# Kernel tuning notes

Measured on AMD Instinct MI355X. Metric: run time of the kernel, lower is better.

The kernel has to match this reference:

```python
import jax, jax.numpy as jnp
import numpy as np

D_MODEL = 1024
D_HEAD = 64
MAX_REL = 8
B, T = 4, 4096


def setup_inputs() -> dict:
    key = jax.random.key(0)
    k1, k2, k3, k4, k5 = jax.random.split(key, 5)
    return {
        "x": jax.random.normal(k1, (B, T, D_MODEL), dtype=jnp.float32),
        "W_q": jax.random.normal(k2, (D_HEAD, D_MODEL), dtype=jnp.float32) * (1.0 / np.sqrt(D_MODEL)),
        "W_k": jax.random.normal(k3, (D_HEAD, D_MODEL), dtype=jnp.float32) * (1.0 / np.sqrt(D_MODEL)),
        "W_v": jax.random.normal(k4, (D_HEAD, D_MODEL), dtype=jnp.float32) * (1.0 / np.sqrt(D_MODEL)),
        "rel_emb": jax.random.normal(k5, (2 * MAX_REL + 1, 1), dtype=jnp.float32),
    }


def reference(x, W_q, W_k, W_v, rel_emb):
    Bb, Tt, _ = x.shape
    scale = jnp.sqrt(jnp.asarray(W_q.shape[0], dtype=x.dtype))
    # projections (Linear: x @ W.T)
    q = jnp.einsum("btd,hd->bth", x, W_q)
    k = jnp.einsum("btd,hd->bth", x, W_k)
    v = jnp.einsum("btd,hd->bth", x, W_v)
    scores = jnp.einsum("bth,bsh->bts", q, k) / scale  # [B,T,T]
    # relative position bias: rel_emb[clip(j-i, -M, M) + M]
    i_idx = jnp.arange(Tt)[:, None]
    j_idx = jnp.arange(Tt)[None, :]
    rel = jnp.clip(j_idx - i_idx, -MAX_REL, MAX_REL) + MAX_REL  # [T,T] int
    rel_bias = rel_emb[rel, 0]  # [T,T]
    scores = scores + rel_bias[None, :, :]
    causal = j_idx <= i_idx  # [T,T] lower-triangular
    scores = jnp.where(causal[None, :, :], scores, -jnp.inf)
    attn = jax.nn.softmax(scores, axis=-1)
    return jnp.einsum("bts,bsh->bth", attn, v)
```

## Files before the change

### kernel.cpp

```cpp
#include <hip/hip_runtime.h>
#include <hip/hip_bf16.h>

#define BT 4
#define TT 4096
#define DM 1024
#define DH 64
#define NRE 17
#define LOG2E 1.4426950408889634f

using bf16 = __hip_bfloat16;
typedef __attribute__((ext_vector_type(8))) short short8;
typedef __attribute__((ext_vector_type(4))) short short4v;
typedef __attribute__((ext_vector_type(4))) float float4v;

#define BC8(x) __builtin_bit_cast(short8, x)

static __device__ __forceinline__ short8 load8(const bf16* p) {
    return *reinterpret_cast<const short8*>(p);
}
static __device__ __forceinline__ short bfbits(float x) {
    return (short)__bfloat16_as_ushort(__float2bfloat16(x));
}
static __device__ __forceinline__ short8 pack8(float4v a, float4v b) {
    short8 r;
    r[0] = bfbits(a[0]); r[1] = bfbits(a[1]); r[2] = bfbits(a[2]); r[3] = bfbits(a[3]);
    r[4] = bfbits(b[0]); r[5] = bfbits(b[1]); r[6] = bfbits(b[2]); r[7] = bfbits(b[3]);
    return r;
}
static __device__ __forceinline__ void gload_lds16(const void* g, void* l) {
    __builtin_amdgcn_global_load_lds(
        (const __attribute__((address_space(1))) void*)g,
        (__attribute__((address_space(3))) void*)l, 16, 0, 0);
}
static __device__ __forceinline__ unsigned lds_addr(const void* p) {
    return (unsigned)(size_t)(const __attribute__((address_space(3))) void*)p;
}

#define DSR(dst, addr, off) \
    asm volatile("ds_read_b128 %0, %1 offset:" off : "=v"(dst) : "v"(addr))


__global__ __launch_bounds__(256) void w_prep(
    const float* __restrict__ Wq, const float* __restrict__ Wk,
    const float* __restrict__ Wv, bf16* __restrict__ Wswz)
{
    const unsigned g = blockIdx.x * 256 + threadIdx.x;
    const unsigned c    = g / 768;
    const unsigned rem  = g - c * 768;
    const unsigned pair = rem >> 3;
    const unsigned slot = rem & 7;
    const unsigned l    = slot ^ (pair & 7);
    const unsigned row  = 2 * pair + (l >> 2);
    const unsigned k    = 32 * c + (l & 3) * 8;
    const float* src = (row < 64) ? &Wq[(size_t)row * DM + k]
                     : (row < 128) ? &Wk[(size_t)(row - 64) * DM + k]
                                   : &Wv[(size_t)(row - 128) * DM + k];
    float4v a = *reinterpret_cast<const float4v*>(src);
    float4v b = *reinterpret_cast<const float4v*>(src + 4);
    *reinterpret_cast<short8*>(&Wswz[(size_t)g * 8]) = pack8(a, b);
}

__global__ __launch_bounds__(256, 2) void qkv_gemm(
    const float* __restrict__ x, const bf16* __restrict__ Wswz,
    bf16* __restrict__ Qb, bf16* __restrict__ Kswz, bf16* __restrict__ Vswz)
{
    __shared__ __align__(16) float xs[2][2048];
    __shared__ __align__(16) short Wls[2][12288];

    const int w    = threadIdx.x >> 6;
    const int lane = threadIdx.x & 63;
    const int quad = lane >> 4;
    const int l16  = lane & 15;
    const int half = w & 1;
    const int colh = w >> 1;
    const int row0 = blockIdx.x * 32;

    float4v acc[6];
#pragma unroll
    for (int i = 0; i < 6; i++) acc[i] = (float4v)(0.f);

    auto stage = [&](int c, int p) {
#pragma unroll
        for (int j = 0; j < 2; j++) {
            const int call = 2 * w + j;
            const int row  = 4 * call + (lane >> 4);
            const int pu   = lane & 15;
            const int gu   = (pu & 8) | ((pu ^ row) & 7);
            gload_lds16(&x[(size_t)(row0 + row) * DM + c * 64 + gu * 4],
                        &xs[p][call * 256]);
        }
#pragma unroll
        for (int j = 0; j < 6; j++) {
            const int call = 6 * w + j;
            gload_lds16(&Wswz[(size_t)(2 * c) * 6144 + call * 512 + lane * 8],
                        &Wls[p][call * 512]);
        }
    };

    const unsigned xlds = lds_addr(&xs[0][0]);
    const unsigned wlds = lds_addr(&Wls[0][0]);
    const int R        = 16 * half + l16;
    const int lo3_0    = (2 * quad)     ^ (R & 7);
    const int lo3_1    = (2 * quad + 1) ^ (R & 7);
    const int pairBase = 48 * colh + (l16 >> 1);
    const int physW    = ((l16 & 1) * 4 + quad) ^ ((l16 >> 1) & 7);

    stage(0, 0);

    for (int c = 0; c < 16; c++) {
        const int p = c & 1;
        __syncthreads();
        if (c + 1 < 16) stage(c + 1, p ^ 1);

        const unsigned xb  = xlds + (unsigned)(p * 8192) + R * 64 * 4;
        const unsigned xa0 = xb + lo3_0 * 16;
        const unsigned xa1 = xb + lo3_1 * 16;
        const unsigned wa  = wlds + (unsigned)(p * 24576) + pairBase * 128 + physW * 16;

        float4v x00, x01, x10, x11;
        float4v w00, w01, w02, w03, w04, w05, w10, w11, w12, w13, w14, w15;
        DSR(x00, xa0, "0");   DSR(x10, xa0, "128");
        DSR(x01, xa1, "0");   DSR(x11, xa1, "128");
        DSR(w00, wa, "0");     DSR(w01, wa, "1024");  DSR(w02, wa, "2048");
        DSR(w03, wa, "3072");  DSR(w04, wa, "4096");  DSR(w05, wa, "5120");
        DSR(w10, wa, "12288"); DSR(w11, wa, "13312"); DSR(w12, wa, "14336");
        DSR(w13, wa, "15360"); DSR(w14, wa, "16384"); DSR(w15, wa, "17408");
        asm volatile("s_waitcnt lgkmcnt(0)"
            : "+v"(x00), "+v"(x01), "+v"(x10), "+v"(x11),
              "+v"(w00), "+v"(w01), "+v"(w02), "+v"(w03), "+v"(w04), "+v"(w05),
              "+v"(w10), "+v"(w11), "+v"(w12), "+v"(w13), "+v"(w14), "+v"(w15));

        short8 a0 = pack8(x00, x01);
        short8 a1 = pack8(x10, x11);
        acc[0] = __builtin_amdgcn_mfma_f32_16x16x32_bf16(a0, BC8(w00), acc[0], 0, 0, 0);
        acc[1] = __builtin_amdgcn_mfma_f32_16x16x32_bf16(a0, BC8(w01), acc[1], 0, 0, 0);
        acc[2] = __builtin_amdgcn_mfma_f32_16x16x32_bf16(a0, BC8(w02), acc[2], 0, 0, 0);
        acc[3] = __builtin_amdgcn_mfma_f32_16x16x32_bf16(a0, BC8(w03), acc[3], 0, 0, 0);
        acc[4] = __builtin_amdgcn_mfma_f32_16x16x32_bf16(a0, BC8(w04), acc[4], 0, 0, 0);
        acc[5] = __builtin_amdgcn_mfma_f32_16x16x32_bf16(a0, BC8(w05), acc[5], 0, 0, 0);
        acc[0] = __builtin_amdgcn_mfma_f32_16x16x32_bf16(a1, BC8(w10), acc[0], 0, 0, 0);
        acc[1] = __builtin_amdgcn_mfma_f32_16x16x32_bf16(a1, BC8(w11), acc[1], 0, 0, 0);
        acc[2] = __builtin_amdgcn_mfma_f32_16x16x32_bf16(a1, BC8(w12), acc[2], 0, 0, 0);
        acc[3] = __builtin_amdgcn_mfma_f32_16x16x32_bf16(a1, BC8(w13), acc[3], 0, 0, 0);
        acc[4] = __builtin_amdgcn_mfma_f32_16x16x32_bf16(a1, BC8(w14), acc[4], 0, 0, 0);
        acc[5] = __builtin_amdgcn_mfma_f32_16x16x32_bf16(a1, BC8(w15), acc[5], 0, 0, 0);
    }

    __syncthreads();
    short* Kimg = (short*)&xs[0][0];
    short* Vimg = Kimg + 2048;
#pragma unroll
    for (int nt = 0; nt < 6; nt++) {
        const int cc = 96 * colh + 16 * nt + l16;
#pragma unroll
        for (int r = 0; r < 4; r++) {
            const int jl = 16 * half + 4 * quad + r;
            const short hb = bfbits(acc[nt][r]);
            if (cc < 64) {
                Qb[(size_t)(row0 + jl) * DH + cc] = __hip_bfloat16_raw{(unsigned short)hb};
            } else if (cc < 128) {
                const int k  = cc - 64;
                const int h  = k >> 5;
                const int q2 = (k & 31) >> 3;
                Kimg[((2 * half + h) * 64 + q2 * 16 + 4 * quad + r) * 8 + (k & 7)] = hb;
            } else {
                const int d  = cc - 128;
                const int dh = d >> 5;
                const int hi = (d >> 4) & 1;
                Vimg[((2 * half + dh) * 64 + quad * 16 + (d & 15)) * 8 + hi * 4 + r] = hb;
            }
        }
    }
    __syncthreads();
    {
        const int b_     = row0 >> 12;
        const int tile32 = (row0 & (TT - 1)) >> 5;
        const size_t base = ((size_t)(b_ * 512 + tile32 * 4)) * 512;
        const int u = threadIdx.x;
        *reinterpret_cast<short8*>(&Kswz[base + (size_t)u * 8]) =
            *reinterpret_cast<const short8*>(&Kimg[u * 8]);
        *reinterpret_cast<short8*>(&Vswz[base + (size_t)u * 8]) =
            *reinterpret_cast<const short8*>(&Vimg[u * 8]);
    }
}

__global__ __launch_bounds__(512, 2) void attn(
    const bf16* __restrict__ Qb, const bf16* __restrict__ Kswz,
    const bf16* __restrict__ Vswz, const float* __restrict__ rel,
    float* __restrict__ out)
{
    __shared__ __align__(16) short sbuf[32768];

    const int w     = threadIdx.x >> 6;
    const int lane  = threadIdx.x & 63;
    const int quad  = lane >> 4;
    const int l16   = lane & 15;
    const int batch = blockIdx.x & 3;
    const int pr    = blockIdx.x >> 2;

    const float SCL = 0.125f * LOG2E;
    float relreg = 0.f;
    if (lane < NRE) relreg = rel[lane] * LOG2E;
    const float rel0 = __shfl(relreg, 0, 64);

    const size_t bbase = (size_t)batch * TT;

    short* mybuf = &sbuf[w * 4096];
    const unsigned sbase = lds_addr(&sbuf[0]) + (unsigned)(w * 8192 + lane * 16);

    float* Osh = (float*)&sbuf[0];
    float* mM  = Osh + 4 * 32 * 68;
    float* lL  = mM + 256;

    auto stageKV = [&](int T) {
        const size_t gb = ((size_t)(batch * 512 + T * 4)) * 512;
#pragma unroll
        for (int j = 0; j < 4; j++)
            gload_lds16(&Kswz[gb + j * 512 + lane * 8], mybuf + j * 512);
#pragma unroll
        for (int j = 0; j < 4; j++)
            gload_lds16(&Vswz[gb + j * 512 + lane * 8], mybuf + 2048 + j * 512);
    };

#pragma unroll 1
    for (int ph = 0; ph < 2; ph++) {
        const int t  = ph ? (127 - pr) : pr;
        const int q0 = 32 * t;

        short8 bq[2][2];
#pragma unroll
        for (int qh = 0; qh < 2; qh++) {
            const bf16* qp = &Qb[(bbase + q0 + 16 * qh + l16) * DH];
            bq[qh][0] = load8(qp + quad * 8);
            bq[qh][1] = load8(qp + 32 + quad * 8);
        }
        __builtin_amdgcn_s_waitcnt(0xF70);

        float4v o[2][4];
#pragma unroll
        for (int qh = 0; qh < 2; qh++)
#pragma unroll
            for (int dt = 0; dt < 4; dt++) o[qh][dt] = (float4v)(0.f);
        float m_st[2] = {-1e30f, -1e30f}, l_st[2] = {0.f, 0.f};

        const int cnt = (t >= w) ? (((t - w) >> 3) + 1) : 0;
        if (cnt > 0) stageKV(w);

        for (int k = 0; k < cnt; k++) {
            const int T = w + 8 * k;
            __builtin_amdgcn_s_waitcnt(0xF70);

            float4v kf0, kf1, kf2, kf3, vf0, vf1, vf2, vf3;
            DSR(kf0, sbase, "0");    DSR(kf1, sbase, "1024");
            DSR(kf2, sbase, "2048"); DSR(kf3, sbase, "3072");
            DSR(vf0, sbase, "4096"); DSR(vf1, sbase, "5120");
            DSR(vf2, sbase, "6144"); DSR(vf3, sbase, "7168");
            asm volatile("s_waitcnt lgkmcnt(0)"
                : "+v"(kf0), "+v"(kf1), "+v"(kf2), "+v"(kf3),
                  "+v"(vf0), "+v"(vf1), "+v"(vf2), "+v"(vf3));

            if (k + 1 < cnt) stageKV(w + 8 * (k + 1));

            const int js = 32 * T;
#pragma unroll
            for (int qh = 0; qh < 2; qh++) {
                float4v st[2];
                st[0] = (float4v)(0.f); st[1] = (float4v)(0.f);
                __builtin_amdgcn_s_setprio(1);
                st[0] = __builtin_amdgcn_mfma_f32_16x16x32_bf16(BC8(kf0), bq[qh][0], st[0], 0, 0, 0);
                st[0] = __builtin_amdgcn_mfma_f32_16x16x32_bf16(BC8(kf1), bq[qh][1], st[0], 0, 0, 0);
                st[1] = __builtin_amdgcn_mfma_f32_16x16x32_bf16(BC8(kf2), bq[qh][0], st[1], 0, 0, 0);
                st[1] = __builtin_amdgcn_mfma_f32_16x16x32_bf16(BC8(kf3), bq[qh][1], st[1], 0, 0, 0);
                __builtin_amdgcn_s_setprio(0);

                const int i_row = q0 + 16 * qh + l16;
                float mcur = -1e30f;
                if (js + 40 <= q0 + 16 * qh) {
#pragma unroll
                    for (int n = 0; n < 2; n++)
#pragma unroll
                        for (int r = 0; r < 4; r++) {
                            float v = st[n][r] * SCL + rel0;
                            st[n][r] = v;
                            mcur = fmaxf(mcur, v);
                        }
                } else {
#pragma unroll
                    for (int n = 0; n < 2; n++) {
                        const int jb = js + 16 * n + 4 * quad;
#pragma unroll
                        for (int r = 0; r < 4; r++) {
                            const int d = jb + r - i_row;
                            int idx = d + 8;
                            idx = idx < 0 ? 0 : (idx > 16 ? 16 : idx);
                            float v = st[n][r] * SCL + __shfl(relreg, idx, 64);
                            v = (d > 0) ? -1e30f : v;
                            st[n][r] = v;
                            mcur = fmaxf(mcur, v);
                        }
                    }
                }

                mcur = fmaxf(mcur, __shfl_xor(mcur, 16, 64));
                mcur = fmaxf(mcur, __shfl_xor(mcur, 32, 64));

                if (__any(mcur > m_st[qh] + 8.f)) {
                    const float mn = fmaxf(m_st[qh], mcur);
                    const float alpha = exp2f(m_st[qh] - mn);
                    m_st[qh] = mn;
                    l_st[qh] *= alpha;
#pragma unroll
                    for (int dt = 0; dt < 4; dt++)
#pragma unroll
                        for (int r = 0; r < 4; r++) o[qh][dt][r] *= alpha;
                }
                const float mn = m_st[qh];

                float lsum = 0.f;
                short4v pb[2];
#pragma unroll
                for (int n = 0; n < 2; n++)
#pragma unroll
                    for (int r = 0; r < 4; r++) {
                        const float e = exp2f(st[n][r] - mn);
                        lsum += e;
                        pb[n][r] = bfbits(e);
                    }
                lsum += __shfl_xor(lsum, 16, 64);
                lsum += __shfl_xor(lsum, 32, 64);
                l_st[qh] += lsum;

                __builtin_amdgcn_s_setprio(1);
#pragma unroll
                for (int n = 0; n < 2; n++) {
#pragma unroll
                    for (int dh = 0; dh < 2; dh++) {
                        const short8 vs = BC8((dh == 0) ? ((n == 0) ? vf0 : vf2)
                                                        : ((n == 0) ? vf1 : vf3));
                        short4v lo, hi;
                        lo[0] = vs[0]; lo[1] = vs[1]; lo[2] = vs[2]; lo[3] = vs[3];
                        hi[0] = vs[4]; hi[1] = vs[5]; hi[2] = vs[6]; hi[3] = vs[7];
                        o[qh][2 * dh]     = __builtin_amdgcn_mfma_f32_16x16x16bf16_1k(lo, pb[n], o[qh][2 * dh], 0, 0, 0);
                        o[qh][2 * dh + 1] = __builtin_amdgcn_mfma_f32_16x16x16bf16_1k(hi, pb[n], o[qh][2 * dh + 1], 0, 0, 0);
                    }
                }
                __builtin_amdgcn_s_setprio(0);
            }
        }

        __syncthreads();
        if (w >= 4) {
            const int slot = w - 4;
#pragma unroll
            for (int qh = 0; qh < 2; qh++) {
                const int row = 16 * qh + l16;
                if (quad == 0) { mM[w * 32 + row] = m_st[qh]; lL[w * 32 + row] = l_st[qh]; }
#pragma unroll
                for (int dt = 0; dt < 4; dt++)
                    *reinterpret_cast<float4v*>(&Osh[(slot * 32 + row) * 68 + 16 * dt + 4 * quad]) = o[qh][dt];
            }
        }
        __syncthreads();
        if (w < 4) {
#pragma unroll
            for (int qh = 0; qh < 2; qh++) {
                const int row = 16 * qh + l16;
                const float mp = mM[(w + 4) * 32 + row], lp = lL[(w + 4) * 32 + row];
                const float M  = fmaxf(m_st[qh], mp);
                const float ea = exp2f(m_st[qh] - M);
                const float eb = exp2f(mp - M);
                const float ln = l_st[qh] * ea + lp * eb;
#pragma unroll
                for (int dt = 0; dt < 4; dt++) {
                    float4v op = *reinterpret_cast<float4v*>(&Osh[(w * 32 + row) * 68 + 16 * dt + 4 * quad]);
#pragma unroll
                    for (int r = 0; r < 4; r++) o[qh][dt][r] = o[qh][dt][r] * ea + op[r] * eb;
                }
                if (quad == 0) { mM[w * 32 + row] = M; lL[w * 32 + row] = ln; }
#pragma unroll
                for (int dt = 0; dt < 4; dt++)
                    *reinterpret_cast<float4v*>(&Osh[(w * 32 + row) * 68 + 16 * dt + 4 * quad]) = o[qh][dt];
            }
        }
        __syncthreads();
        {
            for (int idx = threadIdx.x; idx < 32 * 64; idx += 512) {
                const int row = idx >> 6;
                const int col = idx & 63;
                float M = mM[row];
#pragma unroll
                for (int s = 1; s < 4; s++) M = fmaxf(M, mM[s * 32 + row]);
                float L = 0.f, a = 0.f;
#pragma unroll
                for (int s = 0; s < 4; s++) {
                    const float ex = exp2f(mM[s * 32 + row] - M);
                    L += lL[s * 32 + row] * ex;
                    a += Osh[(s * 32 + row) * 68 + col] * ex;
                }
                out[(bbase + q0 + row) * DH + col] = a / L;
            }
        }
        __syncthreads();
    }
}

extern "C" void kernel_launch(void* const* d_in, const int* in_sizes, int n_in,
                              void* d_out, int out_size, void* d_ws, size_t ws_size,
                              hipStream_t stream)
{
    const float* x   = (const float*)d_in[0];
    const float* Wq  = (const float*)d_in[1];
    const float* Wk  = (const float*)d_in[2];
    const float* Wv  = (const float*)d_in[3];
    const float* rel = (const float*)d_in[4];
    float* out = (float*)d_out;

    bf16* Qb   = (bf16*)d_ws;
    bf16* Kswz = Qb   + (size_t)BT * TT * DH;
    bf16* Vswz = Kswz + (size_t)BT * TT * DH;
    bf16* Wswz = Vswz + (size_t)BT * TT * DH;

    w_prep<<<96, 256, 0, stream>>>(Wq, Wk, Wv, Wswz);
    qkv_gemm<<<512, 256, 0, stream>>>(x, Wswz, Qb, Kswz, Vswz);
    attn<<<256, 512, 0, stream>>>(Qb, Kswz, Vswz, rel, out);
}
```

Before: 147.6 us.

## Split attention KV range across two blocks and merge partials in a new kernel

The attention grid is doubled so that each query tile is handled by two blocks, each covering alternating KV tiles (stride 16 instead of 8). One half writes unnormalized partial output directly to out, the other to a workspace buffer, and both save per-row max and sum. A new merge kernel combines the two halves with log-sum-exp rescaling. This gives more parallelism and better occupancy across CUs, at the cost of an extra kernel launch and extra global traffic for the partials.

```diff
diff --git a/kernel.cpp b/kernel.cpp
--- a/kernel.cpp
+++ b/kernel.cpp
@@ -187,7 +187,7 @@
 __global__ __launch_bounds__(512, 2) void attn(
     const bf16* __restrict__ Qb, const bf16* __restrict__ Kswz,
     const bf16* __restrict__ Vswz, const float* __restrict__ rel,
-    float* __restrict__ out)
+    float* __restrict__ out, float* __restrict__ part1, float* __restrict__ msl)
 {
     __shared__ __align__(16) short sbuf[32768];
 
@@ -196,7 +196,10 @@
     const int quad  = lane >> 4;
     const int l16   = lane & 15;
     const int batch = blockIdx.x & 3;
-    const int pr    = blockIdx.x >> 2;
+    const int rest  = blockIdx.x >> 2;
+    const int pr    = rest >> 1;
+    const int hh    = rest & 1;
+    const int s     = w + 8 * hh;
 
     const float SCL = 0.125f * LOG2E;
     float relreg = 0.f;
@@ -243,11 +246,11 @@
             for (int dt = 0; dt < 4; dt++) o[qh][dt] = (float4v)(0.f);
         float m_st[2] = {-1e30f, -1e30f}, l_st[2] = {0.f, 0.f};
 
-        const int cnt = (t >= w) ? (((t - w) >> 3) + 1) : 0;
-        if (cnt > 0) stageKV(w);
+        const int cnt = (t >= s) ? (((t - s) >> 4) + 1) : 0;
+        if (cnt > 0) stageKV(s);
 
         for (int k = 0; k < cnt; k++) {
-            const int T = w + 8 * k;
+            const int T = s + 16 * k;
             __builtin_amdgcn_s_waitcnt(0xF70);
 
             float4v kf0, kf1, kf2, kf3, vf0, vf1, vf2, vf3;
@@ -259,7 +262,7 @@
                 : "+v"(kf0), "+v"(kf1), "+v"(kf2), "+v"(kf3),
                   "+v"(vf0), "+v"(vf1), "+v"(vf2), "+v"(vf3));
 
-            if (k + 1 < cnt) stageKV(w + 8 * (k + 1));
+            if (k + 1 < cnt) stageKV(s + 16 * (k + 1));
 
             const int js = 32 * T;
 #pragma unroll
@@ -384,23 +387,50 @@
         }
         __syncthreads();
         {
+            const int q = batch * 128 + t;
+            float* ob = hh ? (part1 + (size_t)q * 2048)
+                           : (out + ((size_t)bbase + q0) * DH);
+            float* ml = msl + (size_t)(q * 2 + hh) * 64;
             for (int idx = threadIdx.x; idx < 32 * 64; idx += 512) {
                 const int row = idx >> 6;
                 const int col = idx & 63;
                 float M = mM[row];
 #pragma unroll
-                for (int s = 1; s < 4; s++) M = fmaxf(M, mM[s * 32 + row]);
+                for (int s2 = 1; s2 < 4; s2++) M = fmaxf(M, mM[s2 * 32 + row]);
                 float L = 0.f, a = 0.f;
 #pragma unroll
-                for (int s = 0; s < 4; s++) {
-                    const float ex = exp2f(mM[s * 32 + row] - M);
-                    L += lL[s * 32 + row] * ex;
-                    a += Osh[(s * 32 + row) * 68 + col] * ex;
+                for (int s2 = 0; s2 < 4; s2++) {
+                    const float ex = exp2f(mM[s2 * 32 + row] - M);
+                    L += lL[s2 * 32 + row] * ex;
+                    a += Osh[(s2 * 32 + row) * 68 + col] * ex;
                 }
-                out[(bbase + q0 + row) * DH + col] = a / L;
+                ob[idx] = a;
+                if (col == 0) { ml[row] = M; ml[32 + row] = L; }
             }
         }
         __syncthreads();
+    }
+}
+
+__global__ __launch_bounds__(256) void attn_merge(
+    const float* __restrict__ part1, const float* __restrict__ msl,
+    float* __restrict__ out)
+{
+    const int q = blockIdx.x;
+    const int batch = q >> 7, t = q & 127;
+    float* ob0 = out + ((size_t)batch * TT + t * 32) * DH;
+    const float* o1  = part1 + (size_t)q * 2048;
+    const float* ml0 = msl + (size_t)(q * 2 + 0) * 64;
+    const float* ml1 = msl + (size_t)(q * 2 + 1) * 64;
+    for (int idx = threadIdx.x; idx < 32 * 64; idx += 256) {
+        const int row = idx >> 6;
+        const float m0 = ml0[row], m1 = ml1[row];
+        const float l0 = ml0[32 + row], l1 = ml1[32 + row];
+        const float M  = fmaxf(m0, m1);
+        const float e0 = exp2f(m0 - M), e1 = exp2f(m1 - M);
+        const float den = l0 * e0 + l1 * e1;
+        const float num = ob0[idx] * e0 + o1[idx] * e1;
+        ob0[idx] = num / den;
     }
 }
 
@@ -419,8 +449,11 @@
     bf16* Kswz = Qb   + (size_t)BT * TT * DH;
     bf16* Vswz = Kswz + (size_t)BT * TT * DH;
     bf16* Wswz = Vswz + (size_t)BT * TT * DH;
+    float* part1 = (float*)(Wswz + 24576 * 8);
+    float* msl   = part1 + (size_t)512 * 2048;
 
     w_prep<<<96, 256, 0, stream>>>(Wq, Wk, Wv, Wswz);
     qkv_gemm<<<512, 256, 0, stream>>>(x, Wswz, Qb, Kswz, Vswz);
-    attn<<<256, 512, 0, stream>>>(Qb, Kswz, Vswz, rel, out);
-}
+    attn<<<512, 512, 0, stream>>>(Qb, Kswz, Vswz, rel, out, part1, msl);
+    attn_merge<<<512, 256, 0, stream>>>(part1, msl, out);
+}
```

Result: slower. 163.1 us (+10.5%).

## Load K/V tiles directly into registers and compute row sums via MFMA

Applied to the files above, without the earlier changes.

Drops the LDS staging of K/V tiles and instead loads each wave's K and V fragments straight from global memory into registers, prefetching the next tile right after its last use in the current iteration. The softmax denominator is now accumulated by an extra MFMA against a vector of bf16 ones, and the max reduction's cross-lane shuffles run only when a rescale is triggered. This removes LDS round trips, waitcnts and shuffle-based sum reductions, at the cost of more live registers and global-load latency exposed inside the loop. The row sum now uses bf16-rounded probabilities, which matches what the PV product already uses.

```diff
diff --git a/kernel.cpp b/kernel.cpp
--- a/kernel.cpp
+++ b/kernel.cpp
@@ -189,7 +189,7 @@
     const bf16* __restrict__ Vswz, const float* __restrict__ rel,
     float* __restrict__ out)
 {
-    __shared__ __align__(16) short sbuf[32768];
+    __shared__ __align__(16) float smem[9216];
 
     const int w     = threadIdx.x >> 6;
     const int lane  = threadIdx.x & 63;
@@ -205,22 +205,14 @@
 
     const size_t bbase = (size_t)batch * TT;
 
-    short* mybuf = &sbuf[w * 4096];
-    const unsigned sbase = lds_addr(&sbuf[0]) + (unsigned)(w * 8192 + lane * 16);
-
-    float* Osh = (float*)&sbuf[0];
+    float* Osh = smem;
     float* mM  = Osh + 4 * 32 * 68;
     float* lL  = mM + 256;
 
-    auto stageKV = [&](int T) {
-        const size_t gb = ((size_t)(batch * 512 + T * 4)) * 512;
-#pragma unroll
-        for (int j = 0; j < 4; j++)
-            gload_lds16(&Kswz[gb + j * 512 + lane * 8], mybuf + j * 512);
-#pragma unroll
-        for (int j = 0; j < 4; j++)
-            gload_lds16(&Vswz[gb + j * 512 + lane * 8], mybuf + 2048 + j * 512);
-    };
+    const unsigned loff = (unsigned)lane * 8;
+
+    short4v ones4;
+    ones4[0] = ones4[1] = ones4[2] = ones4[3] = (short)0x3F80;
 
 #pragma unroll 1
     for (int ph = 0; ph < 2; ph++) {
@@ -234,56 +226,56 @@
             bq[qh][0] = load8(qp + quad * 8);
             bq[qh][1] = load8(qp + 32 + quad * 8);
         }
-        __builtin_amdgcn_s_waitcnt(0xF70);
 
         float4v o[2][4];
-#pragma unroll
-        for (int qh = 0; qh < 2; qh++)
+        float4v o_l[2];
+#pragma unroll
+        for (int qh = 0; qh < 2; qh++) {
+            o_l[qh] = (float4v)(0.f);
 #pragma unroll
             for (int dt = 0; dt < 4; dt++) o[qh][dt] = (float4v)(0.f);
-        float m_st[2] = {-1e30f, -1e30f}, l_st[2] = {0.f, 0.f};
+        }
+        float m_st[2] = {-1e30f, -1e30f};
 
         const int cnt = (t >= w) ? (((t - w) >> 3) + 1) : 0;
-        if (cnt > 0) stageKV(w);
+
+        short8 K0, K1, K2, K3, V0, V1, V2, V3;
+        if (cnt > 0) {
+            const bf16* kp = Kswz + ((size_t)(batch * 512 + w * 4)) * 512 + loff;
+            const bf16* vp = Vswz + ((size_t)(batch * 512 + w * 4)) * 512 + loff;
+            K0 = load8(kp);        K1 = load8(kp + 512);
+            K2 = load8(kp + 1024); K3 = load8(kp + 1536);
+            V0 = load8(vp);        V1 = load8(vp + 512);
+            V2 = load8(vp + 1024); V3 = load8(vp + 1536);
+        }
 
         for (int k = 0; k < cnt; k++) {
-            const int T = w + 8 * k;
-            __builtin_amdgcn_s_waitcnt(0xF70);
-
-            float4v kf0, kf1, kf2, kf3, vf0, vf1, vf2, vf3;
-            DSR(kf0, sbase, "0");    DSR(kf1, sbase, "1024");
-            DSR(kf2, sbase, "2048"); DSR(kf3, sbase, "3072");
-            DSR(vf0, sbase, "4096"); DSR(vf1, sbase, "5120");
-            DSR(vf2, sbase, "6144"); DSR(vf3, sbase, "7168");
-            asm volatile("s_waitcnt lgkmcnt(0)"
-                : "+v"(kf0), "+v"(kf1), "+v"(kf2), "+v"(kf3),
-                  "+v"(vf0), "+v"(vf1), "+v"(vf2), "+v"(vf3));
-
-            if (k + 1 < cnt) stageKV(w + 8 * (k + 1));
-
+            const int T  = w + 8 * k;
             const int js = 32 * T;
 #pragma unroll
             for (int qh = 0; qh < 2; qh++) {
                 float4v st[2];
                 st[0] = (float4v)(0.f); st[1] = (float4v)(0.f);
                 __builtin_amdgcn_s_setprio(1);
-                st[0] = __builtin_amdgcn_mfma_f32_16x16x32_bf16(BC8(kf0), bq[qh][0], st[0], 0, 0, 0);
-                st[0] = __builtin_amdgcn_mfma_f32_16x16x32_bf16(BC8(kf1), bq[qh][1], st[0], 0, 0, 0);
-                st[1] = __builtin_amdgcn_mfma_f32_16x16x32_bf16(BC8(kf2), bq[qh][0], st[1], 0, 0, 0);
-                st[1] = __builtin_amdgcn_mfma_f32_16x16x32_bf16(BC8(kf3), bq[qh][1], st[1], 0, 0, 0);
+                st[0] = __builtin_amdgcn_mfma_f32_16x16x32_bf16(K0, bq[qh][0], st[0], 0, 0, 0);
+                st[0] = __builtin_amdgcn_mfma_f32_16x16x32_bf16(K1, bq[qh][1], st[0], 0, 0, 0);
+                st[1] = __builtin_amdgcn_mfma_f32_16x16x32_bf16(K2, bq[qh][0], st[1], 0, 0, 0);
+                st[1] = __builtin_amdgcn_mfma_f32_16x16x32_bf16(K3, bq[qh][1], st[1], 0, 0, 0);
                 __builtin_amdgcn_s_setprio(0);
 
+                if (qh == 1 && k + 1 < cnt) {
+                    const bf16* kp = Kswz + ((size_t)(batch * 512 + (T + 8) * 4)) * 512 + loff;
+                    K0 = load8(kp);        K1 = load8(kp + 512);
+                    K2 = load8(kp + 1024); K3 = load8(kp + 1536);
+                }
+
                 const int i_row = q0 + 16 * qh + l16;
-                float mcur = -1e30f;
                 if (js + 40 <= q0 + 16 * qh) {
 #pragma unroll
                     for (int n = 0; n < 2; n++)
 #pragma unroll
-                        for (int r = 0; r < 4; r++) {
-                            float v = st[n][r] * SCL + rel0;
-                            st[n][r] = v;
-                            mcur = fmaxf(mcur, v);
-                        }
+                        for (int r = 0; r < 4; r++)
+                            st[n][r] = st[n][r] * SCL + rel0;
                 } else {
 #pragma unroll
                     for (int n = 0; n < 2; n++) {
@@ -294,49 +286,45 @@
                             int idx = d + 8;
                             idx = idx < 0 ? 0 : (idx > 16 ? 16 : idx);
                             float v = st[n][r] * SCL + __shfl(relreg, idx, 64);
-                            v = (d > 0) ? -1e30f : v;
-                            st[n][r] = v;
-                            mcur = fmaxf(mcur, v);
+                            st[n][r] = (d > 0) ? -1e30f : v;
                         }
                     }
                 }
 
-                mcur = fmaxf(mcur, __shfl_xor(mcur, 16, 64));
-                mcur = fmaxf(mcur, __shfl_xor(mcur, 32, 64));
-
-                if (__any(mcur > m_st[qh] + 8.f)) {
-                    const float mn = fmaxf(m_st[qh], mcur);
+                const float m01 = fmaxf(fmaxf(st[0][0], st[0][1]), fmaxf(st[0][2], st[0][3]));
+                const float m23 = fmaxf(fmaxf(st[1][0], st[1][1]), fmaxf(st[1][2], st[1][3]));
+                const float mloc = fmaxf(m01, m23);
+
+                if (__any(mloc > m_st[qh] + 8.f)) {
+                    float mrow = fmaxf(mloc, __shfl_xor(mloc, 16, 64));
+                    mrow = fmaxf(mrow, __shfl_xor(mrow, 32, 64));
+                    const float mn = fmaxf(m_st[qh], mrow);
                     const float alpha = exp2f(m_st[qh] - mn);
                     m_st[qh] = mn;
-                    l_st[qh] *= alpha;
 #pragma unroll
                     for (int dt = 0; dt < 4; dt++)
 #pragma unroll
                         for (int r = 0; r < 4; r++) o[qh][dt][r] *= alpha;
+#pragma unroll
+                    for (int r = 0; r < 4; r++) o_l[qh][r] *= alpha;
                 }
                 const float mn = m_st[qh];
 
-                float lsum = 0.f;
                 short4v pb[2];
 #pragma unroll
                 for (int n = 0; n < 2; n++)
 #pragma unroll
-                    for (int r = 0; r < 4; r++) {
-                        const float e = exp2f(st[n][r] - mn);
-                        lsum += e;
-                        pb[n][r] = bfbits(e);
-                    }
-                lsum += __shfl_xor(lsum, 16, 64);
-                lsum += __shfl_xor(lsum, 32, 64);
-                l_st[qh] += lsum;
+                    for (int r = 0; r < 4; r++)
+                        pb[n][r] = bfbits(exp2f(st[n][r] - mn));
 
                 __builtin_amdgcn_s_setprio(1);
 #pragma unroll
                 for (int n = 0; n < 2; n++) {
+                    o_l[qh] = __builtin_amdgcn_mfma_f32_16x16x16bf16_1k(ones4, pb[n], o_l[qh], 0, 0, 0);
 #pragma unroll
                     for (int dh = 0; dh < 2; dh++) {
-                        const short8 vs = BC8((dh == 0) ? ((n == 0) ? vf0 : vf2)
-                                                        : ((n == 0) ? vf1 : vf3));
+                        const short8 vs = (dh == 0) ? ((n == 0) ? V0 : V2)
+                                                    : ((n == 0) ? V1 : V3);
                         short4v lo, hi;
                         lo[0] = vs[0]; lo[1] = vs[1]; lo[2] = vs[2]; lo[3] = vs[3];
                         hi[0] = vs[4]; hi[1] = vs[5]; hi[2] = vs[6]; hi[3] = vs[7];
@@ -345,8 +333,18 @@
                     }
                 }
                 __builtin_amdgcn_s_setprio(0);
+
+                if (qh == 1 && k + 1 < cnt) {
+                    const bf16* vp = Vswz + ((size_t)(batch * 512 + (T + 8) * 4)) * 512 + loff;
+                    V0 = load8(vp);        V1 = load8(vp + 512);
+                    V2 = load8(vp + 1024); V3 = load8(vp + 1536);
+                }
             }
         }
+
+        float l_st[2];
+        l_st[0] = o_l[0][0];
+        l_st[1] = o_l[1][0];
 
         __syncthreads();
         if (w >= 4) {
```

Measured after the change: 144.3 us. 2.2% less time.
